# Kernel tuning notes

Hardware: AMD Instinct MI355X
Metric: run time of the kernel (lower is better)

## Reference

```python
import jax, jax.numpy as jnp
import numpy as np

K = 8        # num capsules
DD = 64      # per-capsule dim (delta_d)
D = K * DD   # 512
T = 16384    # num target nodes (segments)
NB = 100000  # num neighbor nodes
E = 131072   # num edges
ROUIT = 3
BETA = 0.5


def seg_softmax(p, seg, num):
    # softmax over entries sharing the same segment id (axis 0)
    m = jax.lax.stop_gradient(jax.ops.segment_max(p, seg, num_segments=num))
    e = jnp.exp(p - m[seg])
    s = jax.ops.segment_sum(e, seg, num_segments=num)
    return e / s[seg]


def l2norm(x):
    # F.normalize along last axis with eps=1e-12
    n = jnp.sqrt(jnp.sum(x * x, axis=-1, keepdims=True))
    return x / jnp.maximum(n, 1e-12)


def setup_inputs() -> dict:
    key = jax.random.key(0)
    ks = jax.random.split(key, 9)
    return {
        "x_nb": jax.random.normal(ks[0], (NB, 512), dtype=jnp.float32),
        "ppr": jax.random.uniform(ks[1], (E,), dtype=jnp.float32),
        "pca_w": jax.random.normal(ks[2], (512, D), dtype=jnp.float32) * 0.02,
        "pca_b": jnp.zeros((D,), dtype=jnp.float32),
        "mlp_w": jax.random.normal(ks[3], (D, 40), dtype=jnp.float32) * 0.02,
        "mlp_b": jnp.zeros((40,), dtype=jnp.float32),
        "row_idx": jnp.sort(jax.random.randint(ks[4], (E,), 0, T, dtype=jnp.int32)),
        "col_idx": jax.random.randint(ks[5], (E,), 0, NB, dtype=jnp.int32),
        "x_idx": jax.random.randint(ks[6], (T,), 0, NB, dtype=jnp.int32),
    }


def reference(x_nb, ppr, pca_w, pca_b, mlp_w, mlp_b, row_idx, col_idx, x_idx):
    # pca projection + relu
    x = jax.nn.relu(x_nb @ pca_w + pca_b)            # (NB, D)
    # segment softmax of ppr over targets
    ppr = seg_softmax(ppr, row_idx, T)               # (E,)
    # is_xNorm: per-capsule l2 normalization
    x = l2norm(x.reshape(-1, K, DD)).reshape(-1, D)
    z = x[col_idx]                                   # (E, D) gathered neighbors
    zk = z.reshape(-1, K, DD)                        # (E, K, DD)
    # init_mtd == 2: ppr-weighted scatter-sum init
    u = jax.ops.segment_sum(z * ppr[:, None], row_idx, num_segments=T)  # (T, D)
    for it in range(ROUIT):
        uk = u[row_idx].reshape(-1, K, DD)           # (E, K, DD)
        p = jnp.einsum('ekd,ekd->ek', uk, zk)        # (E, K) capsule logits
        # attention == 1: segment softmax then blend with ppr
        p = seg_softmax(p, row_idx, T)
        p = BETA * p + (1.0 - BETA) * ppr[:, None]
        # final segment softmax
        p = seg_softmax(p, row_idx, T)
        u = jax.ops.segment_sum(zk * p[:, :, None], row_idx, num_segments=T)  # (T, K, DD)
        if it < ROUIT - 1:
            u = l2norm(u)
        u = u.reshape(T, D)
    out = jax.nn.relu(u)                             # dropout is identity at eval
    logits = out @ mlp_w + mlp_b                     # (T, nclass)
    return jax.nn.log_softmax(logits, axis=1)
```

## Files before the change

### kernel.cpp

```cpp
#include <hip/hip_runtime.h>
#include <cstdint>
#include <cstddef>

#define NB_N 100000
#define E_N  131072
#define T_N  16384
#define D_N  512
#define NCLS 40
#define NTILES 782
#define CAPR 12

typedef unsigned short u16;
typedef unsigned int   u32;
typedef __attribute__((ext_vector_type(8))) short  short8;
typedef __attribute__((ext_vector_type(4))) float  floatx4;

__device__ __forceinline__ u16 f2bf(float f) {
  u32 u = __float_as_uint(f);
  return (u16)((u + 0x7fffu + ((u >> 16) & 1u)) >> 16);
}
__device__ __forceinline__ void unpack8(uint4 z, float* f) {
  f[0] = __uint_as_float(z.x << 16);
  f[1] = __uint_as_float(z.x & 0xffff0000u);
  f[2] = __uint_as_float(z.y << 16);
  f[3] = __uint_as_float(z.y & 0xffff0000u);
  f[4] = __uint_as_float(z.z << 16);
  f[5] = __uint_as_float(z.z & 0xffff0000u);
  f[6] = __uint_as_float(z.w << 16);
  f[7] = __uint_as_float(z.w & 0xffff0000u);
}
__device__ __forceinline__ void gload_lds16(const void* g, void* s) {
  __builtin_amdgcn_global_load_lds(
      (const __attribute__((address_space(1))) unsigned int*)g,
      (__attribute__((address_space(3))) unsigned int*)s, 16, 0, 0);
}

__global__ void conv_bt(const float* __restrict__ w, u16* __restrict__ Bt) {
  int i = blockIdx.x * 256 + threadIdx.x;
  int n = i >> 9, k = i & 511;
  Bt[i] = f2bf(w[k * 512 + n]);
}

__global__ void conv_bt2(const float* __restrict__ w, u16* __restrict__ Bt2) {
  int i = blockIdx.x * 256 + threadIdx.x;
  int n = i >> 9, k = i & 511;
  Bt2[i] = (n < NCLS) ? f2bf(w[k * NCLS + n]) : (u16)0;
}

__global__ void conv_a(const float* __restrict__ A, u16* __restrict__ Ab) {
  int i = blockIdx.x * 256 + threadIdx.x;
  if (i >= NTILES * 128 * 128) return;
  int row = i >> 7;
  float4 v;
  if (row < NB_N) v = ((const float4*)(A + (size_t)row * 512))[i & 127];
  else            v = make_float4(0.f, 0.f, 0.f, 0.f);
  uint2 pk;
  pk.x = (u32)f2bf(v.x) | ((u32)f2bf(v.y) << 16);
  pk.y = (u32)f2bf(v.z) | ((u32)f2bf(v.w) << 16);
  *(uint2*)(Ab + (size_t)i * 4) = pk;
}

__global__ void build_offs(const int* __restrict__ rowi, int* __restrict__ offs) {
  int e = blockIdx.x * 256 + threadIdx.x;
  if (e >= E_N) return;
  int r  = rowi[e];
  int rp = (e == 0) ? -1 : rowi[e - 1];
  for (int t = rp + 1; t <= r; ++t) offs[t] = e;
  if (e == E_N - 1)
    for (int t = r + 1; t <= T_N; ++t) offs[t] = E_N;
}

__global__ void ppr_sm(const float* __restrict__ ppr, const int* __restrict__ offs,
                       float* __restrict__ pprn) {
  int t = blockIdx.x * 256 + threadIdx.x;
  int s = offs[t], en = offs[t + 1];
  if (s >= en) return;
  float m = -INFINITY;
  for (int e = s; e < en; ++e) m = fmaxf(m, ppr[e]);
  float sum = 0.f;
  for (int e = s; e < en; ++e) sum += expf(ppr[e] - m);
  float inv = 1.f / sum;
  for (int e = s; e < en; ++e) pprn[e] = expf(ppr[e] - m) * inv;
}

__global__ __launch_bounds__(256) void gemm_pca(
    const u16*   __restrict__ Ab,
    const u16*   __restrict__ Bt,
    const float* __restrict__ bias,
    u16*         __restrict__ xn) {
  __shared__ u16 SMEM[2 * 128 * 64];
  u16* As = SMEM;
  u16* Bs = SMEM + 128 * 64;
  const int tid  = threadIdx.x;
  const int wid  = tid >> 6, lane = tid & 63;
  const int quad = lane >> 4, l16 = lane & 15;
  const int b  = blockIdx.x;
  const int mt = (b & 7) | ((b >> 5) << 3);
  if (mt >= NTILES) return;
  const int m0 = mt * 128;
  const int n0 = ((b >> 3) & 3) * 128;
  const int wm = (wid >> 1) * 64;
  const int wn = (wid & 1) * 64;
  const int sw = l16 & 7;
  const u16* Arow = Ab + (size_t)m0 * 512;

  floatx4 acc[4][4];
#pragma unroll
  for (int i = 0; i < 4; ++i)
#pragma unroll
    for (int j = 0; j < 4; ++j) acc[i][j] = (floatx4){0.f, 0.f, 0.f, 0.f};

  for (int k0 = 0; k0 < 512; k0 += 64) {
#pragma unroll
    for (int j = 0; j < 4; ++j) {
      int ci  = j * 256 + wid * 64 + lane;
      int row = ci >> 3;
      int kcs = (lane & 7) ^ ((lane >> 3) & 7);
      gload_lds16(Arow + (size_t)row * 512 + k0 + kcs * 8,
                  &As[(size_t)(j * 256 + wid * 64) * 8]);
      gload_lds16(Bt + (size_t)(n0 + row) * 512 + k0 + kcs * 8,
                  &Bs[(size_t)(j * 256 + wid * 64) * 8]);
    }
    __syncthreads();
#pragma unroll
    for (int kk = 0; kk < 64; kk += 32) {
      short8 af[4], bf[4];
#pragma unroll
      for (int mi = 0; mi < 4; ++mi) {
        int c = (kk >> 3) + quad;
        af[mi] = *(const short8*)(&As[(wm + mi * 16 + l16) * 64 + ((c ^ sw) << 3)]);
      }
#pragma unroll
      for (int ni = 0; ni < 4; ++ni) {
        int c = (kk >> 3) + quad;
        bf[ni] = *(const short8*)(&Bs[(wn + ni * 16 + l16) * 64 + ((c ^ sw) << 3)]);
      }
#pragma unroll
      for (int mi = 0; mi < 4; ++mi)
#pragma unroll
        for (int ni = 0; ni < 4; ++ni)
          acc[mi][ni] = __builtin_amdgcn_mfma_f32_16x16x32_bf16(af[mi], bf[ni],
                                                                acc[mi][ni], 0, 0, 0);
    }
    __syncthreads();
  }

  u16* Os = SMEM;
#pragma unroll
  for (int mi = 0; mi < 4; ++mi) {
#pragma unroll
    for (int r = 0; r < 4; ++r) {
      int lrow = wm + mi * 16 + quad * 4 + r;
      float v[4];
      float ss = 0.f;
#pragma unroll
      for (int ni = 0; ni < 4; ++ni) {
        int n  = n0 + wn + ni * 16 + l16;
        float x = acc[mi][ni][r] + bias[n];
        x = fmaxf(x, 0.f);
        v[ni] = x;
        ss += x * x;
      }
      ss += __shfl_xor(ss, 1);
      ss += __shfl_xor(ss, 2);
      ss += __shfl_xor(ss, 4);
      ss += __shfl_xor(ss, 8);
      float sc = 1.f / fmaxf(sqrtf(ss), 1e-12f);
#pragma unroll
      for (int ni = 0; ni < 4; ++ni)
        Os[lrow * 128 + wn + ni * 16 + l16] = f2bf(v[ni] * sc);
    }
  }
  __syncthreads();
#pragma unroll
  for (int c8 = 0; c8 < 8; ++c8) {
    int idx = c8 * 256 + tid;
    int row = idx >> 4, chk = idx & 15;
    int gm = m0 + row;
    if (gm < NB_N) {
      uint4 val = *(const uint4*)(&Os[row * 128 + chk * 8]);
      *(uint4*)(xn + (size_t)gm * 512 + n0 + chk * 8) = val;
    }
  }
}

__device__ __forceinline__ void matvec16(const float (&g0)[16], const float (&g1)[16],
                                         float w0, float w1, int base,
                                         float& e0, float& e1) {
  e0 = 0.f; e1 = 0.f;
#pragma unroll
  for (int j = 0; j < 8; ++j) {
    float wj = __shfl(w0, base | j);
    e0 += g0[j] * wj;
    e1 += g1[j] * wj;
  }
#pragma unroll
  for (int j = 0; j < 8; ++j) {
    float wj = __shfl(w1, base | j);
    e0 += g0[8 + j] * wj;
    e1 += g1[8 + j] * wj;
  }
}

__device__ __forceinline__ void segsm2(float& d0, float& d1, bool v0, bool v1) {
  float m = fmaxf(v0 ? d0 : -INFINITY, v1 ? d1 : -INFINITY);
  m = fmaxf(m, __shfl_xor(m, 1));
  m = fmaxf(m, __shfl_xor(m, 2));
  m = fmaxf(m, __shfl_xor(m, 4));
  float e0 = v0 ? expf(d0 - m) : 0.f;
  float e1 = v1 ? expf(d1 - m) : 0.f;
  float s = e0 + e1;
  s += __shfl_xor(s, 1);
  s += __shfl_xor(s, 2);
  s += __shfl_xor(s, 4);
  float inv = 1.f / s;
  d0 = e0 * inv;
  d1 = e1 * inv;
}

__global__ __launch_bounds__(128, 4) void fused_all(
    const u16* __restrict__ xn, const int* __restrict__ coli,
    const int* __restrict__ offs, const float* __restrict__ pprn,
    u16* __restrict__ ub) {
  __shared__ __align__(16) float Glds[2][8 * 260];
  const int lane = threadIdx.x & 63;
  const int wv = threadIdx.x >> 6;
  const int t = blockIdx.x * 2 + wv;
  const int s = offs[t], en = offs[t + 1];
  int deg = en - s;
  if (deg > 64) deg = 64;

  int   mycol = (lane < deg) ? coli[s + lane] : 0;
  float myppr = (lane < deg) ? pprn[s + lane] : 0.f;

  float uf[8] = {0.f, 0.f, 0.f, 0.f, 0.f, 0.f, 0.f, 0.f};

  if (deg <= 16) {
    float* G = Glds[wv];
    const int esrc = lane & 15, kq = lane >> 4;
    int ce = __shfl(mycol, esrc);
    const u16* zb = xn + (size_t)ce * 512 + kq * 8;
    floatx4 gram[8];
#pragma unroll
    for (int c = 0; c < 8; ++c) {
      short8 f0 = *(const short8*)(zb + c * 64);
      short8 f1 = *(const short8*)(zb + c * 64 + 32);
      floatx4 gg = (floatx4){0.f, 0.f, 0.f, 0.f};
      gg = __builtin_amdgcn_mfma_f32_16x16x32_bf16(f0, f0, gg, 0, 0, 0);
      gg = __builtin_amdgcn_mfma_f32_16x16x32_bf16(f1, f1, gg, 0, 0, 0);
      gram[c] = gg;
    }
#pragma unroll
    for (int c = 0; c < 8; ++c)
      *(float4*)&G[c * 260 + esrc * 16 + kq * 4] = *(float4*)&gram[c];
    const int cc = lane >> 3, i0 = lane & 7;
    const int base = lane & 56;
    float g0[16], g1[16];
    {
      const float* r0 = &G[cc * 260 + i0 * 16];
      const float* r1 = &G[cc * 260 + (i0 + 8) * 16];
#pragma unroll
      for (int ch = 0; ch < 4; ++ch) {
        float4 a = *(const float4*)(r0 + ch * 4);
        float4 b = *(const float4*)(r1 + ch * 4);
        g0[ch * 4 + 0] = a.x; g0[ch * 4 + 1] = a.y;
        g0[ch * 4 + 2] = a.z; g0[ch * 4 + 3] = a.w;
        g1[ch * 4 + 0] = b.x; g1[ch * 4 + 1] = b.y;
        g1[ch * 4 + 2] = b.z; g1[ch * 4 + 3] = b.w;
      }
    }
    const bool v0 = i0 < deg, v1 = (i0 + 8) < deg;
    float pr0 = __shfl(myppr, i0);
    float pr1 = __shfl(myppr, i0 + 8);

    float d0, d1;
    matvec16(g0, g1, pr0, pr1, base, d0, d1);

    float w0 = 0.f, w1 = 0.f;
#pragma unroll
    for (int it = 0; it < 3; ++it) {
      segsm2(d0, d1, v0, v1);
      d0 = 0.5f * d0 + 0.5f * pr0;
      d1 = 0.5f * d1 + 0.5f * pr1;
      segsm2(d0, d1, v0, v1);
      w0 = d0; w1 = d1;
      if (it < 2) {
        float e0, e1;
        matvec16(g0, g1, w0, w1, base, e0, e1);
        float nv = w0 * e0 + w1 * e1;
        nv += __shfl_xor(nv, 1);
        nv += __shfl_xor(nv, 2);
        nv += __shfl_xor(nv, 4);
        float invn = 1.f / fmaxf(sqrtf(nv), 1e-12f);
        d0 = e0 * invn;
        d1 = e1 * invn;
      }
    }

#pragma unroll
    for (int j = 0; j < 16; ++j) {
      if (j < deg) {
        float wj = __shfl((j < 8) ? w0 : w1, base | (j & 7));
        int cj = __shfl(mycol, j);
        uint4 zz = *(const uint4*)(xn + (size_t)cj * 512 + lane * 8);
        float zf[8];
        unpack8(zz, zf);
#pragma unroll
        for (int q = 0; q < 8; ++q) uf[q] += wj * zf[q];
      }
    }
  } else {
    const int cap = lane >> 3;
    const int slot = lane >> 3;

    uint4 zreg[CAPR];
#pragma unroll
    for (int j = 0; j < CAPR; ++j) {
      if (j < deg) {
        int c = __shfl(mycol, j);
        zreg[j] = *(const uint4*)(xn + (size_t)c * 512 + lane * 8);
      }
    }

#pragma unroll
    for (int j = 0; j < CAPR; ++j) {
      if (j < deg) {
        float w = __shfl(myppr, j);
        float zf[8];
        unpack8(zreg[j], zf);
#pragma unroll
        for (int q = 0; q < 8; ++q) uf[q] += w * zf[q];
      }
    }
    for (int j = CAPR; j < deg; ++j) {
      float w = __shfl(myppr, j);
      int c = __shfl(mycol, j);
      uint4 zz = *(const uint4*)(xn + (size_t)c * 512 + lane * 8);
      float zf[8];
      unpack8(zz, zf);
#pragma unroll
      for (int q = 0; q < 8; ++q) uf[q] += w * zf[q];
    }

    float Preg[8];

    for (int it = 0; it < 3; ++it) {
#pragma unroll
      for (int j = 0; j < CAPR; ++j) {
        if (j < deg) {
          float zf[8];
          unpack8(zreg[j], zf);
          float d = uf[0]*zf[0] + uf[1]*zf[1] + uf[2]*zf[2] + uf[3]*zf[3] +
                    uf[4]*zf[4] + uf[5]*zf[5] + uf[6]*zf[6] + uf[7]*zf[7];
          d += __shfl_xor(d, 1);
          d += __shfl_xor(d, 2);
          d += __shfl_xor(d, 4);
          float dc = __shfl(d, (lane & 7) << 3);
          if (slot == (j & 7)) Preg[j >> 3] = dc;
        }
      }
      for (int j = CAPR; j < deg; ++j) {
        int c = __shfl(mycol, j);
        uint4 zz = *(const uint4*)(xn + (size_t)c * 512 + lane * 8);
        float zf[8];
        unpack8(zz, zf);
        float d = uf[0]*zf[0] + uf[1]*zf[1] + uf[2]*zf[2] + uf[3]*zf[3] +
                  uf[4]*zf[4] + uf[5]*zf[5] + uf[6]*zf[6] + uf[7]*zf[7];
        d += __shfl_xor(d, 1);
        d += __shfl_xor(d, 2);
        d += __shfl_xor(d, 4);
        float dc = __shfl(d, (lane & 7) << 3);
        if (slot == (j & 7)) {
          int hi = j >> 3;
          if      (hi == 1) Preg[1] = dc;
          else if (hi == 2) Preg[2] = dc;
          else if (hi == 3) Preg[3] = dc;
          else if (hi == 4) Preg[4] = dc;
          else if (hi == 5) Preg[5] = dc;
          else if (hi == 6) Preg[6] = dc;
          else if (hi == 7) Preg[7] = dc;
        }
      }

      {
        float m1 = -INFINITY;
#pragma unroll
        for (int i = 0; i < 8; ++i)
          m1 = (slot + 8*i < deg) ? fmaxf(m1, Preg[i]) : m1;
        m1 = fmaxf(m1, __shfl_xor(m1, 8));
        m1 = fmaxf(m1, __shfl_xor(m1, 16));
        m1 = fmaxf(m1, __shfl_xor(m1, 32));
        float s1 = 0.f;
#pragma unroll
        for (int i = 0; i < 8; ++i)
          s1 += (slot + 8*i < deg) ? expf(Preg[i] - m1) : 0.f;
        s1 += __shfl_xor(s1, 8);
        s1 += __shfl_xor(s1, 16);
        s1 += __shfl_xor(s1, 32);
        float inv1 = 1.f / s1;
        float m2 = -INFINITY;
#pragma unroll
        for (int i = 0; i < 8; ++i) {
          int j = slot + 8*i;
          if (j < deg) {
            float pj = __shfl(myppr, j);
            float v = 0.5f * expf(Preg[i] - m1) * inv1 + 0.5f * pj;
            Preg[i] = v;
            m2 = fmaxf(m2, v);
          }
        }
        m2 = fmaxf(m2, __shfl_xor(m2, 8));
        m2 = fmaxf(m2, __shfl_xor(m2, 16));
        m2 = fmaxf(m2, __shfl_xor(m2, 32));
        float s2 = 0.f;
#pragma unroll
        for (int i = 0; i < 8; ++i)
          s2 += (slot + 8*i < deg) ? expf(Preg[i] - m2) : 0.f;
        s2 += __shfl_xor(s2, 8);
        s2 += __shfl_xor(s2, 16);
        s2 += __shfl_xor(s2, 32);
        float inv2 = 1.f / s2;
#pragma unroll
        for (int i = 0; i < 8; ++i)
          if (slot + 8*i < deg) Preg[i] = expf(Preg[i] - m2) * inv2;
      }

      float acc[8] = {0.f, 0.f, 0.f, 0.f, 0.f, 0.f, 0.f, 0.f};
#pragma unroll
      for (int j = 0; j < CAPR; ++j) {
        if (j < deg) {
          float w = __shfl(Preg[j >> 3], ((j & 7) << 3) | cap);
          float zf[8];
          unpack8(zreg[j], zf);
#pragma unroll
          for (int q = 0; q < 8; ++q) acc[q] += w * zf[q];
        }
      }
      for (int j = CAPR; j < deg; ++j) {
        int hi = j >> 3;
        float pr = Preg[1];
        if      (hi == 2) pr = Preg[2];
        else if (hi == 3) pr = Preg[3];
        else if (hi == 4) pr = Preg[4];
        else if (hi == 5) pr = Preg[5];
        else if (hi == 6) pr = Preg[6];
        else if (hi == 7) pr = Preg[7];
        float w = __shfl(pr, ((j & 7) << 3) | cap);
        int c = __shfl(mycol, j);
        uint4 zz = *(const uint4*)(xn + (size_t)c * 512 + lane * 8);
        float zf[8];
        unpack8(zz, zf);
#pragma unroll
        for (int q = 0; q < 8; ++q) acc[q] += w * zf[q];
      }
      if (it < 2) {
        float ss = 0.f;
#pragma unroll
        for (int q = 0; q < 8; ++q) ss += acc[q] * acc[q];
        ss += __shfl_xor(ss, 1);
        ss += __shfl_xor(ss, 2);
        ss += __shfl_xor(ss, 4);
        float sc = 1.f / fmaxf(sqrtf(ss), 1e-12f);
#pragma unroll
        for (int q = 0; q < 8; ++q) acc[q] *= sc;
      }
#pragma unroll
      for (int q = 0; q < 8; ++q) uf[q] = acc[q];
    }
  }

  uint4 pk;
  pk.x = (u32)f2bf(fmaxf(uf[0], 0.f)) | ((u32)f2bf(fmaxf(uf[1], 0.f)) << 16);
  pk.y = (u32)f2bf(fmaxf(uf[2], 0.f)) | ((u32)f2bf(fmaxf(uf[3], 0.f)) << 16);
  pk.z = (u32)f2bf(fmaxf(uf[4], 0.f)) | ((u32)f2bf(fmaxf(uf[5], 0.f)) << 16);
  pk.w = (u32)f2bf(fmaxf(uf[6], 0.f)) | ((u32)f2bf(fmaxf(uf[7], 0.f)) << 16);
  *(uint4*)(ub + (size_t)t * 512 + lane * 8) = pk;
}

__global__ __launch_bounds__(256) void mlp_gemm(
    const u16* __restrict__ ub, const u16* __restrict__ Bt2,
    const float* __restrict__ mb, float* __restrict__ out) {
  const int wid = threadIdx.x >> 6, lane = threadIdx.x & 63;
  const int quad = lane >> 4, l16 = lane & 15;
  const int m0 = blockIdx.x * 64 + wid * 16;

  floatx4 acc[4];
#pragma unroll
  for (int ni = 0; ni < 4; ++ni) acc[ni] = (floatx4){0.f, 0.f, 0.f, 0.f};

#pragma unroll 4
  for (int kk = 0; kk < 512; kk += 32) {
    short8 af = *(const short8*)(ub + (size_t)(m0 + l16) * 512 + kk + quad * 8);
#pragma unroll
    for (int ni = 0; ni < 4; ++ni) {
      short8 bf = *(const short8*)(Bt2 + (size_t)(ni * 16 + l16) * 512 + kk + quad * 8);
      acc[ni] = __builtin_amdgcn_mfma_f32_16x16x32_bf16(af, bf, acc[ni], 0, 0, 0);
    }
  }

#pragma unroll
  for (int r = 0; r < 4; ++r) {
    int t = m0 + quad * 4 + r;
    float v[4];
    float mx = -INFINITY;
#pragma unroll
    for (int ni = 0; ni < 4; ++ni) {
      int c = ni * 16 + l16;
      float lg = (c < NCLS) ? (acc[ni][r] + mb[c]) : -INFINITY;
      v[ni] = lg;
      mx = fmaxf(mx, lg);
    }
    mx = fmaxf(mx, __shfl_xor(mx, 1));
    mx = fmaxf(mx, __shfl_xor(mx, 2));
    mx = fmaxf(mx, __shfl_xor(mx, 4));
    mx = fmaxf(mx, __shfl_xor(mx, 8));
    float se = 0.f;
#pragma unroll
    for (int ni = 0; ni < 4; ++ni) {
      int c = ni * 16 + l16;
      if (c < NCLS) se += expf(v[ni] - mx);
    }
    se += __shfl_xor(se, 1);
    se += __shfl_xor(se, 2);
    se += __shfl_xor(se, 4);
    se += __shfl_xor(se, 8);
    float lse = mx + logf(se);
#pragma unroll
    for (int ni = 0; ni < 4; ++ni) {
      int c = ni * 16 + l16;
      if (c < NCLS) out[(size_t)t * NCLS + c] = v[ni] - lse;
    }
  }
}

extern "C" void kernel_launch(void* const* d_in, const int* in_sizes, int n_in,
                              void* d_out, int out_size, void* d_ws, size_t ws_size,
                              hipStream_t stream) {
  const float* x_nb  = (const float*)d_in[0];
  const float* ppr   = (const float*)d_in[1];
  const float* pca_w = (const float*)d_in[2];
  const float* pca_b = (const float*)d_in[3];
  const float* mlp_w = (const float*)d_in[4];
  const float* mlp_b = (const float*)d_in[5];
  const int* row_idx = (const int*)d_in[6];
  const int* col_idx = (const int*)d_in[7];
  float* out = (float*)d_out;

  char* ws = (char*)d_ws;
  const size_t OFF_BT   = 0;
  const size_t OFF_PPRN = 512 * 1024;
  const size_t OFF_OFFS = 1024 * 1024;
  const size_t OFF_XN   = 1024 * 1024 + 128 * 1024;
  const size_t OFF_AB   = OFF_XN + (size_t)NB_N * 512 * 2;
  const size_t OFF_UB   = OFF_AB + (size_t)NTILES * 128 * 512 * 2;
  u16*   Bt   = (u16*)(ws + OFF_BT);
  u16*   Bt2  = (u16*)(ws + OFF_BT);
  float* pprn = (float*)(ws + OFF_PPRN);
  int*   offs = (int*)(ws + OFF_OFFS);
  u16*   xn   = (u16*)(ws + OFF_XN);
  u16*   Ab   = (u16*)(ws + OFF_AB);
  u16*   ub   = (u16*)(ws + OFF_UB);

  conv_bt<<<1024, 256, 0, stream>>>(pca_w, Bt);
  build_offs<<<512, 256, 0, stream>>>(row_idx, offs);
  ppr_sm<<<64, 256, 0, stream>>>(ppr, offs, pprn);

  conv_a<<<(NTILES * 128 * 128 + 255) / 256, 256, 0, stream>>>(x_nb, Ab);
  gemm_pca<<<98 * 32, 256, 0, stream>>>(Ab, Bt, pca_b, xn);
  conv_bt2<<<128, 256, 0, stream>>>(mlp_w, Bt2);

  fused_all<<<T_N / 2, 128, 0, stream>>>(xn, col_idx, offs, pprn, ub);

  mlp_gemm<<<256, 256, 0, stream>>>(ub, Bt2, mlp_b, out);
}
```

Baseline: 507.1 us.

## Fuse fp32-to-bf16 conversion of input into PCA GEMM A-tile loads

Removes the separate conv_a kernel that wrote a bf16 copy of x_nb. The GEMM now reads fp32 rows directly, converts them with v_cvt_pk_bf16_f32 and stores them into swizzled LDS. The aim is to save a full write and re-read of roughly 100 MB of bf16 staging data. In exchange the A loads become synchronous register loads instead of async global_load_lds, and launch bounds add an occupancy hint of 3.

Measured after the change: 515.7 us. No clear change (+1.7%).

```diff
diff --git a/kernel.cpp b/kernel.cpp
--- a/kernel.cpp
+++ b/kernel.cpp
@@ -34,6 +34,11 @@
       (const __attribute__((address_space(1))) unsigned int*)g,
       (__attribute__((address_space(3))) unsigned int*)s, 16, 0, 0);
 }
+__device__ __forceinline__ u32 cvtpk_bf16(float lo, float hi) {
+  u32 r;
+  asm("v_cvt_pk_bf16_f32 %0, %1, %2" : "=v"(r) : "v"(lo), "v"(hi));
+  return r;
+}
 
 __global__ void conv_bt(const float* __restrict__ w, u16* __restrict__ Bt) {
   int i = blockIdx.x * 256 + threadIdx.x;
@@ -45,19 +50,6 @@
   int i = blockIdx.x * 256 + threadIdx.x;
   int n = i >> 9, k = i & 511;
   Bt2[i] = (n < NCLS) ? f2bf(w[k * NCLS + n]) : (u16)0;
-}
-
-__global__ void conv_a(const float* __restrict__ A, u16* __restrict__ Ab) {
-  int i = blockIdx.x * 256 + threadIdx.x;
-  if (i >= NTILES * 128 * 128) return;
-  int row = i >> 7;
-  float4 v;
-  if (row < NB_N) v = ((const float4*)(A + (size_t)row * 512))[i & 127];
-  else            v = make_float4(0.f, 0.f, 0.f, 0.f);
-  uint2 pk;
-  pk.x = (u32)f2bf(v.x) | ((u32)f2bf(v.y) << 16);
-  pk.y = (u32)f2bf(v.z) | ((u32)f2bf(v.w) << 16);
-  *(uint2*)(Ab + (size_t)i * 4) = pk;
 }
 
 __global__ void build_offs(const int* __restrict__ rowi, int* __restrict__ offs) {
@@ -83,8 +75,8 @@
   for (int e = s; e < en; ++e) pprn[e] = expf(ppr[e] - m) * inv;
 }
 
-__global__ __launch_bounds__(256) void gemm_pca(
-    const u16*   __restrict__ Ab,
+__global__ __launch_bounds__(256, 3) void gemm_pca(
+    const float* __restrict__ A,
     const u16*   __restrict__ Bt,
     const float* __restrict__ bias,
     u16*         __restrict__ xn) {
@@ -102,7 +94,6 @@
   const int wm = (wid >> 1) * 64;
   const int wn = (wid & 1) * 64;
   const int sw = l16 & 7;
-  const u16* Arow = Ab + (size_t)m0 * 512;
 
   floatx4 acc[4][4];
 #pragma unroll
@@ -116,10 +107,28 @@
       int ci  = j * 256 + wid * 64 + lane;
       int row = ci >> 3;
       int kcs = (lane & 7) ^ ((lane >> 3) & 7);
-      gload_lds16(Arow + (size_t)row * 512 + k0 + kcs * 8,
-                  &As[(size_t)(j * 256 + wid * 64) * 8]);
       gload_lds16(Bt + (size_t)(n0 + row) * 512 + k0 + kcs * 8,
                   &Bs[(size_t)(j * 256 + wid * 64) * 8]);
+    }
+#pragma unroll
+    for (int j = 0; j < 4; ++j) {
+      int ci  = j * 256 + tid;
+      int row = ci >> 3, kc = ci & 7;
+      int gm  = m0 + row;
+      float4 v0 = make_float4(0.f, 0.f, 0.f, 0.f);
+      float4 v1 = make_float4(0.f, 0.f, 0.f, 0.f);
+      if (gm < NB_N) {
+        const float* src = A + (size_t)gm * 512 + k0 + kc * 8;
+        v0 = *(const float4*)(src);
+        v1 = *(const float4*)(src + 4);
+      }
+      uint4 pk;
+      pk.x = cvtpk_bf16(v0.x, v0.y);
+      pk.y = cvtpk_bf16(v0.z, v0.w);
+      pk.z = cvtpk_bf16(v1.x, v1.y);
+      pk.w = cvtpk_bf16(v1.z, v1.w);
+      int dc = kc ^ (row & 7);
+      *(uint4*)(&As[(size_t)(row * 8 + dc) * 8]) = pk;
     }
     __syncthreads();
 #pragma unroll
@@ -548,26 +557,24 @@
 
   char* ws = (char*)d_ws;
   const size_t OFF_BT   = 0;
-  const size_t OFF_PPRN = 512 * 1024;
-  const size_t OFF_OFFS = 1024 * 1024;
-  const size_t OFF_XN   = 1024 * 1024 + 128 * 1024;
-  const size_t OFF_AB   = OFF_XN + (size_t)NB_N * 512 * 2;
-  const size_t OFF_UB   = OFF_AB + (size_t)NTILES * 128 * 512 * 2;
+  const size_t OFF_BT2  = 512 * 1024;
+  const size_t OFF_PPRN = 640 * 1024;
+  const size_t OFF_OFFS = 1152 * 1024;
+  const size_t OFF_XN   = 1280 * 1024;
+  const size_t OFF_UB   = OFF_XN + (size_t)NB_N * 512 * 2;
   u16*   Bt   = (u16*)(ws + OFF_BT);
-  u16*   Bt2  = (u16*)(ws + OFF_BT);
+  u16*   Bt2  = (u16*)(ws + OFF_BT2);
   float* pprn = (float*)(ws + OFF_PPRN);
   int*   offs = (int*)(ws + OFF_OFFS);
   u16*   xn   = (u16*)(ws + OFF_XN);
-  u16*   Ab   = (u16*)(ws + OFF_AB);
   u16*   ub   = (u16*)(ws + OFF_UB);
 
   conv_bt<<<1024, 256, 0, stream>>>(pca_w, Bt);
+  conv_bt2<<<128, 256, 0, stream>>>(mlp_w, Bt2);
   build_offs<<<512, 256, 0, stream>>>(row_idx, offs);
   ppr_sm<<<64, 256, 0, stream>>>(ppr, offs, pprn);
 
-  conv_a<<<(NTILES * 128 * 128 + 255) / 256, 256, 0, stream>>>(x_nb, Ab);
-  gemm_pca<<<98 * 32, 256, 0, stream>>>(Ab, Bt, pca_b, xn);
-  conv_bt2<<<128, 256, 0, stream>>>(mlp_w, Bt2);
+  gemm_pca<<<98 * 32, 256, 0, stream>>>(x_nb, Bt, pca_b, xn);
 
   fused_all<<<T_N / 2, 128, 0, stream>>>(xn, col_idx, offs, pprn, ub);
 
```
